# Optimization experiments

Hardware: AMD Instinct MI355X
Metric: run time of the kernel (lower is better)

Reference implementation:

```python
import jax, jax.numpy as jnp
import numpy as np

D_IN = 1024
D_OUT = 1024
NUM_HEADS = 16
HEAD_DIM = D_OUT // NUM_HEADS


def setup_inputs() -> dict:
    key = jax.random.key(0)
    k_x, k_qkv, k_pw, k_pb = jax.random.split(key, 4)
    x = jax.random.normal(k_x, (2, 2048, D_IN), dtype=jnp.float32)
    # torch nn.Linear(d_in, 3*d_out, bias=False): weight [3*d_out, d_in]
    w_qkv = jax.random.normal(k_qkv, (3 * D_OUT, D_IN), dtype=jnp.float32) * (1.0 / np.sqrt(D_IN))
    # proj: nn.Linear(d_out, d_out) with bias
    w_proj = jax.random.normal(k_pw, (D_OUT, D_OUT), dtype=jnp.float32) * (1.0 / np.sqrt(D_OUT))
    b_proj = jax.random.normal(k_pb, (D_OUT,), dtype=jnp.float32) * 0.01
    return {"x": x, "w_qkv": w_qkv, "w_proj": w_proj, "b_proj": b_proj}


def reference(x, w_qkv, w_proj, b_proj):
    B, S, _ = x.shape
    # fused QKV projection: [B,S,3*D_OUT]
    qkv = jnp.einsum('bsd,ed->bse', x, w_qkv)
    qkv = qkv.reshape(B, S, 3, NUM_HEADS, HEAD_DIM)
    q, k, v = jnp.moveaxis(qkv, 2, 0)  # each [B,S,H,Dh]
    scale = 1.0 / jnp.sqrt(jnp.asarray(HEAD_DIM, dtype=x.dtype))
    # scores [B,H,S,S]
    scores = jnp.einsum('bqhd,bkhd->bhqk', q, k) * scale
    causal = jnp.tril(jnp.ones((S, S), dtype=bool))
    scores = jnp.where(causal, scores, jnp.asarray(-jnp.inf, dtype=scores.dtype))
    attn = jax.nn.softmax(scores, axis=-1)
    ctx = jnp.einsum('bhqk,bkhd->bqhd', attn, v)  # [B,S,H,Dh]
    ctx = ctx.reshape(B, S, D_OUT)
    return jnp.einsum('bsd,ed->bse', ctx, w_proj) + b_proj
```

## Files before the change

### kernel.cpp

```cpp
#include <hip/hip_runtime.h>
#include <hip/hip_bf16.h>
#include <cstdint>

#define B_SZ   2
#define S_LEN  2048
#define NH     16
#define LDA    72

using f32x4 = __attribute__((ext_vector_type(4))) float;
typedef __bf16 bf16x8 __attribute__((ext_vector_type(8)));
typedef __bf16 bf16x4 __attribute__((ext_vector_type(4)));

__device__ inline float bf2f(unsigned short u) {
    union { unsigned int i; float f; } v; v.i = ((unsigned int)u) << 16; return v.f;
}
__device__ inline unsigned short f2bf(float f) {
    union { float f; unsigned int i; } v; v.f = f;
    unsigned int r = v.i + 0x7fff + ((v.i >> 16) & 1);
    return (unsigned short)(r >> 16);
}
__device__ inline f32x4 mfma16(bf16x8 a, bf16x8 b, f32x4 c) {
    return __builtin_amdgcn_mfma_f32_16x16x32_bf16(a, b, c, 0, 0, 0);
}
__device__ inline void stC(float* C, size_t idx, float v)  { C[idx] = v; }
__device__ inline void stC(__bf16* C, size_t idx, float v) { ((unsigned short*)C)[idx] = f2bf(v); }

__global__ __launch_bounds__(256) void f2b_kernel(
    const float* __restrict__ in, __bf16* __restrict__ out, int n4)
{
    int i = blockIdx.x * blockDim.x + threadIdx.x;
    if (i < n4) {
        float4 v = ((const float4*)in)[i];
        ushort4 o;
        o.x = f2bf(v.x); o.y = f2bf(v.y); o.z = f2bf(v.z); o.w = f2bf(v.w);
        ((ushort4*)out)[i] = o;
    }
}

template <typename TO, int HAS_BIAS>
__global__ __launch_bounds__(256) void gemm128(
    const __bf16* __restrict__ A, const __bf16* __restrict__ W,
    const float* __restrict__ bias, TO* __restrict__ C,
    int M, int N, int K)
{
    __shared__ __bf16 Alds[128 * 32];
    __shared__ __bf16 Blds[128 * 32];
    const int tid  = threadIdx.x, lane = tid & 63, w = tid >> 6;
    const int c16  = lane & 15, quad = lane >> 4;
    const int mBase = blockIdx.y * 128, nBase = blockIdx.x * 128;
    const int moff = (w & 1) * 64, noff = (w >> 1) * 64;

    f32x4 acc[4][4];
#pragma unroll
    for (int i = 0; i < 4; ++i)
#pragma unroll
        for (int j = 0; j < 4; ++j) acc[i][j] = (f32x4){0.f, 0.f, 0.f, 0.f};

    for (int k0 = 0; k0 < K; k0 += 32) {
        __syncthreads();
#pragma unroll
        for (int p = 0; p < 2; ++p) {
            const int linear = p * 256 + tid;
            const int row = linear >> 2;
            const int seg = (linear & 3) ^ (row & 3);
            const int lbase = (p * 256 + w * 64) * 8;
            const __bf16* ga = A + (size_t)(mBase + row) * K + k0 + seg * 8;
            const __bf16* gb = W + (size_t)(nBase + row) * K + k0 + seg * 8;
            __builtin_amdgcn_global_load_lds(
                (const __attribute__((address_space(1))) void*)ga,
                (__attribute__((address_space(3))) void*)(Alds + lbase), 16, 0, 0);
            __builtin_amdgcn_global_load_lds(
                (const __attribute__((address_space(1))) void*)gb,
                (__attribute__((address_space(3))) void*)(Blds + lbase), 16, 0, 0);
        }
        __syncthreads();

        bf16x8 af[4], bw[4];
#pragma unroll
        for (int i = 0; i < 4; ++i) {
            const int rowA = moff + i * 16 + c16;
            af[i] = *(const bf16x8*)&Alds[rowA * 32 + ((quad ^ (rowA & 3)) << 3)];
            const int rowB = noff + i * 16 + c16;
            bw[i] = *(const bf16x8*)&Blds[rowB * 32 + ((quad ^ (rowB & 3)) << 3)];
        }
#pragma unroll
        for (int i = 0; i < 4; ++i)
#pragma unroll
            for (int j = 0; j < 4; ++j)
                acc[i][j] = mfma16(af[i], bw[j], acc[i][j]);
    }

#pragma unroll
    for (int j = 0; j < 4; ++j) {
        const int col = nBase + noff + j * 16 + c16;
        const float bv = HAS_BIAS ? bias[col] : 0.f;
#pragma unroll
        for (int i = 0; i < 4; ++i)
#pragma unroll
            for (int r = 0; r < 4; ++r) {
                const int row = mBase + moff + i * 16 + quad * 4 + r;
                stC(C, (size_t)row * N + col, acc[i][j][r] + bv);
            }
    }
}

__global__ __launch_bounds__(256) void attn(
    const __bf16* __restrict__ qkv, __bf16* __restrict__ ctx)
{
    __shared__ __bf16 Qs[64 * LDA];
    __shared__ __bf16 Ks[64 * LDA];
    __shared__ __bf16 Vs[64 * LDA];
    __shared__ __bf16 Ps[64 * LDA];

    const int tid  = threadIdx.x;
    const int lane = tid & 63;
    const int w    = tid >> 6;
    const int c16  = lane & 15;
    const int quad = lane >> 4;
    const int bh = blockIdx.x, b = bh >> 4, h = bh & 15;
    const int qt = (int)gridDim.y - 1 - (int)blockIdx.y;
    const int qBase = qt * 64;

    const float QS = 0.125f * 1.4426950408889634f;

#pragma unroll
    for (int p = 0; p < 2; ++p) {
        const int linear = p * 256 + tid;
        const int row = linear >> 3;
        const int d0 = (linear & 7) * 8;
        const __bf16* g = qkv + (size_t)(b * S_LEN + qBase + row) * 3072 + h * 64 + d0;
        uint4 raw = *(const uint4*)g;
        const unsigned short* u = (const unsigned short*)&raw;
        unsigned short tmp[8];
#pragma unroll
        for (int jj = 0; jj < 8; ++jj) tmp[jj] = f2bf(bf2f(u[jj]) * QS);
        *(uint4*)&Qs[row * LDA + d0] = *(const uint4*)tmp;
    }
    __syncthreads();

    const bf16x8 aq0 = *(const bf16x8*)&Qs[(w * 16 + c16) * LDA + quad * 8];
    const bf16x8 aq1 = *(const bf16x8*)&Qs[(w * 16 + c16) * LDA + 32 + quad * 8];

    float l_r[4] = {0.f, 0.f, 0.f, 0.f};
    f32x4 acc_o[4];
#pragma unroll
    for (int j = 0; j < 4; ++j) acc_o[j] = (f32x4){0.f, 0.f, 0.f, 0.f};

    const int nCh = qt + 1;
    for (int cc = 0; cc < nCh; ++cc) {
        const int kBase = cc * 64;
#pragma unroll
        for (int p = 0; p < 2; ++p) {
            const int linear = p * 256 + tid;
            const int row = linear >> 3;
            const int d0 = (linear & 7) * 8;
            const __bf16* g = qkv + (size_t)(b * S_LEN + kBase + row) * 3072 + 1024 + h * 64 + d0;
            uint4 raw = *(const uint4*)g;
            *(uint4*)&Ks[row * LDA + d0] = raw;
        }
        {
            const int c16t = tid & 15;
            const int jh   = (tid >> 4) & 1;
            const int dblk = tid >> 5;
            const int key1 = (2 * jh) * 16 + c16t;
            const __bf16* g1 = qkv + (size_t)(b * S_LEN + kBase + key1) * 3072 + 2048 + h * 64 + dblk * 8;
            const __bf16* g2 = g1 + 16 * 3072;
            uint4 r1 = *(const uint4*)g1;
            uint4 r2 = *(const uint4*)g2;
            const unsigned short* e1 = (const unsigned short*)&r1;
            const unsigned short* e2 = (const unsigned short*)&r2;
#pragma unroll
            for (int d = 0; d < 8; ++d) {
                const unsigned pack = (unsigned)e1[d] | ((unsigned)e2[d] << 16);
                *(unsigned*)&Vs[(dblk * 8 + d) * LDA + c16t * 4 + 2 * jh] = pack;
            }
        }
        __syncthreads();

        f32x4 sc[4];
#pragma unroll
        for (int j = 0; j < 4; ++j) sc[j] = (f32x4){0.f, 0.f, 0.f, 0.f};
#pragma unroll
        for (int j = 0; j < 4; ++j) {
            bf16x8 bk0 = *(const bf16x8*)&Ks[(j * 16 + c16) * LDA + quad * 8];
            bf16x8 bk1 = *(const bf16x8*)&Ks[(j * 16 + c16) * LDA + 32 + quad * 8];
            sc[j] = mfma16(aq0, bk0, sc[j]);
            sc[j] = mfma16(aq1, bk1, sc[j]);
        }

        if (cc == nCh - 1) {
#pragma unroll
            for (int j = 0; j < 4; ++j) {
                const int key = kBase + j * 16 + c16;
#pragma unroll
                for (int r = 0; r < 4; ++r) {
                    const int q = qBase + w * 16 + quad * 4 + r;
                    if (key > q) sc[j][r] = -1e30f;
                }
            }
        }

        float p_[4][4];
#pragma unroll
        for (int j = 0; j < 4; ++j)
#pragma unroll
            for (int r = 0; r < 4; ++r)
                p_[j][r] = exp2f(sc[j][r]);
#pragma unroll
        for (int r = 0; r < 4; ++r)
            l_r[r] += (p_[0][r] + p_[1][r]) + (p_[2][r] + p_[3][r]);

#pragma unroll
        for (int r = 0; r < 4; ++r) {
            bf16x4 pb;
            pb[0] = (__bf16)p_[0][r]; pb[1] = (__bf16)p_[1][r];
            pb[2] = (__bf16)p_[2][r]; pb[3] = (__bf16)p_[3][r];
            *(bf16x4*)&Ps[(w * 16 + quad * 4 + r) * LDA + c16 * 4] = pb;
        }

        bf16x8 ap0 = *(const bf16x8*)&Ps[(w * 16 + c16) * LDA + quad * 8];
        bf16x8 ap1 = *(const bf16x8*)&Ps[(w * 16 + c16) * LDA + 32 + quad * 8];
#pragma unroll
        for (int j = 0; j < 4; ++j) {
            bf16x8 bv0 = *(const bf16x8*)&Vs[(j * 16 + c16) * LDA + quad * 8];
            bf16x8 bv1 = *(const bf16x8*)&Vs[(j * 16 + c16) * LDA + 32 + quad * 8];
            acc_o[j] = mfma16(ap0, bv0, acc_o[j]);
            acc_o[j] = mfma16(ap1, bv1, acc_o[j]);
        }
        __syncthreads();
    }

#pragma unroll
    for (int r = 0; r < 4; ++r) {
        float l = l_r[r];
        l += __shfl_xor(l, 1);
        l += __shfl_xor(l, 2);
        l += __shfl_xor(l, 4);
        l += __shfl_xor(l, 8);
        const float inv = 1.0f / l;
        const size_t rowO = (size_t)(b * S_LEN + qBase + w * 16 + quad * 4 + r) * 1024 + h * 64;
#pragma unroll
        for (int j = 0; j < 4; ++j)
            ctx[rowO + j * 16 + c16] = (__bf16)(acc_o[j][r] * inv);
    }
}

extern "C" void kernel_launch(void* const* d_in, const int* in_sizes, int n_in,
                              void* d_out, int out_size, void* d_ws, size_t ws_size,
                              hipStream_t stream) {
    const float* x      = (const float*)d_in[0];
    const float* w_qkv  = (const float*)d_in[1];
    const float* w_proj = (const float*)d_in[2];
    const float* b_proj = (const float*)d_in[3];
    float* out = (float*)d_out;

    __bf16* qkvb = (__bf16*)d_ws;
    __bf16* xb   = qkvb + (size_t)4096 * 3072;
    __bf16* wqb  = xb + (size_t)4096 * 1024;
    __bf16* ctxb = xb;
    __bf16* wpb  = wqb;

    const int M = B_SZ * S_LEN;

    f2b_kernel<<<(4096 * 1024 / 4 + 255) / 256, 256, 0, stream>>>(x, xb, 4096 * 1024 / 4);
    f2b_kernel<<<(3072 * 1024 / 4 + 255) / 256, 256, 0, stream>>>(w_qkv, wqb, 3072 * 1024 / 4);

    gemm128<__bf16, 0><<<dim3(3072 / 128, M / 128), 256, 0, stream>>>(
        xb, wqb, nullptr, qkvb, M, 3072, 1024);

    attn<<<dim3(B_SZ * NH, S_LEN / 64), 256, 0, stream>>>(qkvb, ctxb);

    f2b_kernel<<<(1024 * 1024 / 4 + 255) / 256, 256, 0, stream>>>(w_proj, wpb, 1024 * 1024 / 4);

    gemm128<float, 1><<<dim3(1024 / 128, M / 128), 256, 0, stream>>>(
        ctxb, wpb, b_proj, out, M, 1024, 1024);
}
```

Baseline: 208.7 us.

## Double-buffer GEMM LDS tiles and register-prefetch K/V chunks in attention

The GEMM now uses two LDS buffers per operand and issues the global-to-LDS loads for the next K slice before computing on the current one, leaving one barrier per iteration. The attention kernel loads the next K/V chunk into registers right after the barrier, so those global loads overlap the QK^T, softmax and PV work, and then writes them to LDS at the top of the next iteration. Both changes aim to hide global memory latency behind MFMA work. The cost is double the GEMM LDS footprint and more registers in attention, which may lower occupancy.

```diff
diff --git a/kernel.cpp b/kernel.cpp
--- a/kernel.cpp
+++ b/kernel.cpp
@@ -43,8 +43,8 @@
     const float* __restrict__ bias, TO* __restrict__ C,
     int M, int N, int K)
 {
-    __shared__ __bf16 Alds[128 * 32];
-    __shared__ __bf16 Blds[128 * 32];
+    __shared__ __bf16 Alds[2][128 * 32];
+    __shared__ __bf16 Blds[2][128 * 32];
     const int tid  = threadIdx.x, lane = tid & 63, w = tid >> 6;
     const int c16  = lane & 15, quad = lane >> 4;
     const int mBase = blockIdx.y * 128, nBase = blockIdx.x * 128;
@@ -56,8 +56,7 @@
 #pragma unroll
         for (int j = 0; j < 4; ++j) acc[i][j] = (f32x4){0.f, 0.f, 0.f, 0.f};
 
-    for (int k0 = 0; k0 < K; k0 += 32) {
-        __syncthreads();
+    auto stage = [&](int buf, int k0) {
 #pragma unroll
         for (int p = 0; p < 2; ++p) {
             const int linear = p * 256 + tid;
@@ -68,26 +67,33 @@
             const __bf16* gb = W + (size_t)(nBase + row) * K + k0 + seg * 8;
             __builtin_amdgcn_global_load_lds(
                 (const __attribute__((address_space(1))) void*)ga,
-                (__attribute__((address_space(3))) void*)(Alds + lbase), 16, 0, 0);
+                (__attribute__((address_space(3))) void*)(&Alds[buf][lbase]), 16, 0, 0);
             __builtin_amdgcn_global_load_lds(
                 (const __attribute__((address_space(1))) void*)gb,
-                (__attribute__((address_space(3))) void*)(Blds + lbase), 16, 0, 0);
-        }
+                (__attribute__((address_space(3))) void*)(&Blds[buf][lbase]), 16, 0, 0);
+        }
+    };
+
+    stage(0, 0);
+    int cur = 0;
+    for (int k0 = 0; k0 < K; k0 += 32) {
         __syncthreads();
+        if (k0 + 32 < K) stage(cur ^ 1, k0 + 32);
 
         bf16x8 af[4], bw[4];
 #pragma unroll
         for (int i = 0; i < 4; ++i) {
             const int rowA = moff + i * 16 + c16;
-            af[i] = *(const bf16x8*)&Alds[rowA * 32 + ((quad ^ (rowA & 3)) << 3)];
+            af[i] = *(const bf16x8*)&Alds[cur][rowA * 32 + ((quad ^ (rowA & 3)) << 3)];
             const int rowB = noff + i * 16 + c16;
-            bw[i] = *(const bf16x8*)&Blds[rowB * 32 + ((quad ^ (rowB & 3)) << 3)];
+            bw[i] = *(const bf16x8*)&Blds[cur][rowB * 32 + ((quad ^ (rowB & 3)) << 3)];
         }
 #pragma unroll
         for (int i = 0; i < 4; ++i)
 #pragma unroll
             for (int j = 0; j < 4; ++j)
                 acc[i][j] = mfma16(af[i], bw[j], acc[i][j]);
+        cur ^= 1;
     }
 
 #pragma unroll
@@ -123,6 +129,22 @@
 
     const float QS = 0.125f * 1.4426950408889634f;
 
+    const int krow0 = tid >> 3;
+    const int kd0   = (tid & 7) * 8;
+    const int c16t = tid & 15;
+    const int jh   = (tid >> 4) & 1;
+    const int dblk = tid >> 5;
+
+    uint4 kreg[2], vreg[2];
+    auto loadKV = [&](int kBase) {
+        const size_t base = (size_t)(b * S_LEN + kBase) * 3072 + h * 64;
+        kreg[0] = *(const uint4*)(qkv + base + (size_t)krow0 * 3072 + 1024 + kd0);
+        kreg[1] = *(const uint4*)(qkv + base + (size_t)(krow0 + 32) * 3072 + 1024 + kd0);
+        const __bf16* g1 = qkv + base + (size_t)(2 * jh * 16 + c16t) * 3072 + 2048 + dblk * 8;
+        vreg[0] = *(const uint4*)g1;
+        vreg[1] = *(const uint4*)(g1 + (size_t)16 * 3072);
+    };
+
 #pragma unroll
     for (int p = 0; p < 2; ++p) {
         const int linear = p * 256 + tid;
@@ -136,6 +158,7 @@
         for (int jj = 0; jj < 8; ++jj) tmp[jj] = f2bf(bf2f(u[jj]) * QS);
         *(uint4*)&Qs[row * LDA + d0] = *(const uint4*)tmp;
     }
+    loadKV(0);
     __syncthreads();
 
     const bf16x8 aq0 = *(const bf16x8*)&Qs[(w * 16 + c16) * LDA + quad * 8];
@@ -148,27 +171,11 @@
 
     const int nCh = qt + 1;
     for (int cc = 0; cc < nCh; ++cc) {
-        const int kBase = cc * 64;
-#pragma unroll
-        for (int p = 0; p < 2; ++p) {
-            const int linear = p * 256 + tid;
-            const int row = linear >> 3;
-            const int d0 = (linear & 7) * 8;
-            const __bf16* g = qkv + (size_t)(b * S_LEN + kBase + row) * 3072 + 1024 + h * 64 + d0;
-            uint4 raw = *(const uint4*)g;
-            *(uint4*)&Ks[row * LDA + d0] = raw;
-        }
+        *(uint4*)&Ks[krow0 * LDA + kd0]        = kreg[0];
+        *(uint4*)&Ks[(krow0 + 32) * LDA + kd0] = kreg[1];
         {
-            const int c16t = tid & 15;
-            const int jh   = (tid >> 4) & 1;
-            const int dblk = tid >> 5;
-            const int key1 = (2 * jh) * 16 + c16t;
-            const __bf16* g1 = qkv + (size_t)(b * S_LEN + kBase + key1) * 3072 + 2048 + h * 64 + dblk * 8;
-            const __bf16* g2 = g1 + 16 * 3072;
-            uint4 r1 = *(const uint4*)g1;
-            uint4 r2 = *(const uint4*)g2;
-            const unsigned short* e1 = (const unsigned short*)&r1;
-            const unsigned short* e2 = (const unsigned short*)&r2;
+            const unsigned short* e1 = (const unsigned short*)&vreg[0];
+            const unsigned short* e2 = (const unsigned short*)&vreg[1];
 #pragma unroll
             for (int d = 0; d < 8; ++d) {
                 const unsigned pack = (unsigned)e1[d] | ((unsigned)e2[d] << 16);
@@ -176,6 +183,7 @@
             }
         }
         __syncthreads();
+        if (cc + 1 < nCh) loadKV((cc + 1) * 64);
 
         f32x4 sc[4];
 #pragma unroll
@@ -191,7 +199,7 @@
         if (cc == nCh - 1) {
 #pragma unroll
             for (int j = 0; j < 4; ++j) {
-                const int key = kBase + j * 16 + c16;
+                const int key = cc * 64 + j * 16 + c16;
 #pragma unroll
                 for (int r = 0; r < 4; ++r) {
                     const int q = qBase + w * 16 + quad * 4 + r;
```

After: 212.8 us. Within noise of the previous version (+1.9%).
